# Performance work log

Hardware: AMD Instinct MI355X
Metric: run time of the kernel (lower is better)

## Reference

```python
import jax, jax.numpy as jnp
import numpy as np

B, C, H, W = 4, 256, 64, 64
N = H * W


def setup_inputs() -> dict:
    key = jax.random.key(0)
    k1, k2, k3, k4, k5 = jax.random.split(key, 5)
    energy = jax.random.normal(k1, (B, N, N), dtype=jnp.float32)
    x = jax.random.normal(k2, (B, C, H, W), dtype=jnp.float32)
    # 1x1 conv params (kernel is [C_out, C_in] after squeezing the 1x1 spatial dims)
    fan = 1.0 / np.sqrt(C)
    value_w = jax.random.uniform(k3, (C, C), dtype=jnp.float32, minval=-fan, maxval=fan)
    value_b = jax.random.uniform(k4, (C,), dtype=jnp.float32, minval=-fan, maxval=fan)
    # nn.Parameter(torch.zeros(1)) -> use small random scalar so output is non-trivial
    gamma = jax.random.normal(k5, (1,), dtype=jnp.float32) * 0.1
    return {"energy": energy, "x": x, "value_w": value_w, "value_b": value_b, "gamma": gamma}


def reference(energy, x, value_w, value_b, gamma):
    # softmax over last dim of the [B, N, N] score matrix (dropout in eval mode = identity)
    attention = jax.nn.softmax(energy, axis=-1)  # [B, N, N]
    # 1x1 conv: per-pixel channel mixing
    value = jnp.einsum('bchw,oc->bohw', x, value_w) + value_b[None, :, None, None]
    value = value.reshape(x.shape[0], -1, N)  # [B, C, N]
    # out[b,c,m] = sum_n value[b,c,n] * attention[b,m,n]  (bmm with attention^T)
    out = jnp.einsum('bcn,bmn->bcm', value, attention)
    out = out.reshape(x.shape)  # [B, C, H, W]
    return gamma[0] * out + 2.0 * x
```

## Files before the change

### kernel.cpp

```cpp
#include <hip/hip_runtime.h>

#define Bb 4
#define Cc 256
#define Nn 4096

typedef __attribute__((ext_vector_type(8))) short bf16x8;
typedef __attribute__((ext_vector_type(4))) float f32x4;

__device__ __forceinline__ unsigned short f2bf(float f) {
    union { float f; unsigned u; } v; v.f = f;
    unsigned r = v.u + 0x7FFF + ((v.u >> 16) & 1);
    return (unsigned short)(r >> 16);
}

__device__ __forceinline__ void async_copy16(const void* g, void* l) {
    __builtin_amdgcn_global_load_lds(
        (const __attribute__((address_space(1))) unsigned int*)g,
        (__attribute__((address_space(3))) unsigned int*)l, 16, 0, 0);
}

__global__ __launch_bounds__(256) void value_gemm(
    const float* __restrict__ X, const float* __restrict__ W,
    const float* __restrict__ bias, unsigned short* __restrict__ Vout)
{
    __shared__ unsigned short a_lds[128 * 32];
    __shared__ unsigned short b_lds[128 * 32];

    const int t = threadIdx.x;
    const int blk = blockIdx.x;
    const int b  = blk >> 6;
    const int r  = blk & 63;
    const int o0 = (r >> 5) * 128;
    const int n0 = (r & 31) * 128;

    const int wave = t >> 6, lane = t & 63;
    const int wm = wave >> 1, wn = wave & 1;
    const int lrow = lane & 15, lq = lane >> 4;

    f32x4 acc[4][4] = {};

    for (int c0 = 0; c0 < Cc; c0 += 32) {
        __syncthreads();
        #pragma unroll
        for (int k = 0; k < 4; ++k) {
            const int idx = t + 256 * k;
            const int row = idx >> 3, c4 = idx & 7;
            const float4 v = *(const float4*)&W[(size_t)(o0 + row) * Cc + c0 + c4 * 4];
            ushort4 h; h.x = f2bf(v.x); h.y = f2bf(v.y); h.z = f2bf(v.z); h.w = f2bf(v.w);
            *(ushort4*)&a_lds[row * 32 + c4 * 4] = h;
        }
        #pragma unroll
        for (int k = 0; k < 4; ++k) {
            const int idx = t + 256 * k;
            const int rc = idx >> 5, n4 = idx & 31;
            const float4 v = *(const float4*)&X[((size_t)(b * Cc + c0 + rc)) * Nn + n0 + n4 * 4];
            b_lds[(n4 * 4 + 0) * 32 + rc] = f2bf(v.x);
            b_lds[(n4 * 4 + 1) * 32 + rc] = f2bf(v.y);
            b_lds[(n4 * 4 + 2) * 32 + rc] = f2bf(v.z);
            b_lds[(n4 * 4 + 3) * 32 + rc] = f2bf(v.w);
        }
        __syncthreads();

        bf16x8 af[4], bfr[4];
        #pragma unroll
        for (int i = 0; i < 4; ++i)
            af[i] = *(const bf16x8*)&a_lds[(wm * 64 + i * 16 + lrow) * 32 + lq * 8];
        #pragma unroll
        for (int i = 0; i < 4; ++i)
            bfr[i] = *(const bf16x8*)&b_lds[(wn * 64 + i * 16 + lrow) * 32 + lq * 8];
        #pragma unroll
        for (int mi = 0; mi < 4; ++mi)
            #pragma unroll
            for (int ni = 0; ni < 4; ++ni)
                acc[mi][ni] = __builtin_amdgcn_mfma_f32_16x16x32_bf16(
                    af[mi], bfr[ni], acc[mi][ni], 0, 0, 0);
    }

    #pragma unroll
    for (int mi = 0; mi < 4; ++mi) {
        #pragma unroll
        for (int ni = 0; ni < 4; ++ni) {
            #pragma unroll
            for (int rr = 0; rr < 4; ++rr) {
                const int o = o0 + wm * 64 + mi * 16 + lq * 4 + rr;
                const int n = n0 + wn * 64 + ni * 16 + lrow;
                Vout[((size_t)(b * Cc + o)) * Nn + n] = f2bf(acc[mi][ni][rr] + bias[o]);
            }
        }
    }
}

__global__ __launch_bounds__(256) void attn_gemm(
    const unsigned short* __restrict__ V, const float* __restrict__ E,
    const float* __restrict__ X, const float* __restrict__ gamma,
    float* __restrict__ Out)
{
    __shared__ unsigned short a_lds[128 * 32];
    __shared__ unsigned short b_lds[128 * 32];
    __shared__ float sum_lds[128];

    const int t = threadIdx.x;
    const int blk = blockIdx.x;
    const int b  = blk >> 6;
    const int r  = blk & 63;
    const int c0 = (r >> 5) * 128;
    const int m0 = (r & 31) * 128;

    const int wave = t >> 6, lane = t & 63;
    const int wm = wave >> 1, wn = wave & 1;
    const int lrow = lane & 15, lq = lane >> 4;

    f32x4 acc[4][4] = {};
    float sacc[4] = {0.f, 0.f, 0.f, 0.f};

    const int arow0 = t >> 2;
    const int acol  = (t & 3) * 8;

    for (int k0 = 0; k0 < Nn; k0 += 32) {
        __syncthreads();
        async_copy16(&V[((size_t)(b * Cc + c0 + arow0)) * Nn + k0 + acol],
                     &a_lds[(size_t)t * 8]);
        async_copy16(&V[((size_t)(b * Cc + c0 + 64 + arow0)) * Nn + k0 + acol],
                     &a_lds[(size_t)(t + 256) * 8]);
        #pragma unroll
        for (int k = 0; k < 4; ++k) {
            const int idx = t + 256 * k;
            const int rowm = idx >> 3, n4 = idx & 7;
            const float4 e = *(const float4*)&E[((size_t)b * Nn + m0 + rowm) * Nn + k0 + n4 * 4];
            const float e0 = __expf(e.x), e1 = __expf(e.y), e2 = __expf(e.z), e3 = __expf(e.w);
            sacc[k] += (e0 + e1) + (e2 + e3);
            ushort4 h; h.x = f2bf(e0); h.y = f2bf(e1); h.z = f2bf(e2); h.w = f2bf(e3);
            *(ushort4*)&b_lds[rowm * 32 + n4 * 4] = h;
        }
        __syncthreads();

        bf16x8 af[4], bfr[4];
        #pragma unroll
        for (int i = 0; i < 4; ++i)
            af[i] = *(const bf16x8*)&a_lds[(wm * 64 + i * 16 + lrow) * 32 + lq * 8];
        #pragma unroll
        for (int i = 0; i < 4; ++i)
            bfr[i] = *(const bf16x8*)&b_lds[(wn * 64 + i * 16 + lrow) * 32 + lq * 8];
        #pragma unroll
        for (int mi = 0; mi < 4; ++mi)
            #pragma unroll
            for (int ni = 0; ni < 4; ++ni)
                acc[mi][ni] = __builtin_amdgcn_mfma_f32_16x16x32_bf16(
                    af[mi], bfr[ni], acc[mi][ni], 0, 0, 0);
    }

    #pragma unroll
    for (int k = 0; k < 4; ++k) {
        float s = sacc[k];
        s += __shfl_xor(s, 1);
        s += __shfl_xor(s, 2);
        s += __shfl_xor(s, 4);
        if ((t & 7) == 0) sum_lds[(t >> 3) + 32 * k] = s;
    }
    __syncthreads();

    const float g = gamma[0];
    #pragma unroll
    for (int ni = 0; ni < 4; ++ni) {
        const int mloc = wn * 64 + ni * 16 + lrow;
        const float scale = g / sum_lds[mloc];
        const int m = m0 + mloc;
        #pragma unroll
        for (int mi = 0; mi < 4; ++mi) {
            #pragma unroll
            for (int rr = 0; rr < 4; ++rr) {
                const int c = c0 + wm * 64 + mi * 16 + lq * 4 + rr;
                const size_t off = ((size_t)(b * Cc + c)) * Nn + m;
                Out[off] = scale * acc[mi][ni][rr] + 2.0f * X[off];
            }
        }
    }
}

extern "C" void kernel_launch(void* const* d_in, const int* in_sizes, int n_in,
                              void* d_out, int out_size, void* d_ws, size_t ws_size,
                              hipStream_t stream) {
    const float* energy  = (const float*)d_in[0];
    const float* x       = (const float*)d_in[1];
    const float* value_w = (const float*)d_in[2];
    const float* value_b = (const float*)d_in[3];
    const float* gamma   = (const float*)d_in[4];
    float* out = (float*)d_out;
    unsigned short* Vws = (unsigned short*)d_ws;

    value_gemm<<<256, 256, 0, stream>>>(x, value_w, value_b, Vws);
    attn_gemm<<<256, 256, 0, stream>>>(Vws, energy, x, gamma, out);
}
```

Measured before the change: 501.2 us.

## Read energy once per block with full-channel tiles and register-prefetched V pipeline

The attention GEMM now assigns each 512-thread block all 256 channels for 64 output rows, so the large energy matrix is read and exponentiated only once instead of once per channel tile. V fragments are prefetched from global memory directly into registers two steps ahead, and exp'd energy goes into a double-buffered, XOR-swizzled LDS tile with a single barrier per iteration. The value GEMM uses a 64-deep K step with swizzled LDS and smaller output tiles. Trade-offs are higher register pressure and repeated V reads from L2 across blocks.

```diff
diff --git a/kernel.cpp b/kernel.cpp
--- a/kernel.cpp
+++ b/kernel.cpp
@@ -13,165 +13,222 @@
     return (unsigned short)(r >> 16);
 }
 
-__device__ __forceinline__ void async_copy16(const void* g, void* l) {
-    __builtin_amdgcn_global_load_lds(
-        (const __attribute__((address_space(1))) unsigned int*)g,
-        (__attribute__((address_space(3))) unsigned int*)l, 16, 0, 0);
-}
-
 __global__ __launch_bounds__(256) void value_gemm(
     const float* __restrict__ X, const float* __restrict__ W,
     const float* __restrict__ bias, unsigned short* __restrict__ Vout)
 {
-    __shared__ unsigned short a_lds[128 * 32];
-    __shared__ unsigned short b_lds[128 * 32];
+    __shared__ unsigned short a_lds[128 * 64];
+    __shared__ unsigned short b_lds[64 * 64];
 
     const int t = threadIdx.x;
-    const int blk = blockIdx.x;
-    const int b  = blk >> 6;
-    const int r  = blk & 63;
-    const int o0 = (r >> 5) * 128;
-    const int n0 = (r & 31) * 128;
+    const int b  = blockIdx.x >> 7;
+    const int r  = blockIdx.x & 127;
+    const int o0 = (r >> 6) << 7;
+    const int n0 = (r & 63) << 6;
 
     const int wave = t >> 6, lane = t & 63;
     const int wm = wave >> 1, wn = wave & 1;
     const int lrow = lane & 15, lq = lane >> 4;
 
-    f32x4 acc[4][4] = {};
-
-    for (int c0 = 0; c0 < Cc; c0 += 32) {
-        __syncthreads();
-        #pragma unroll
-        for (int k = 0; k < 4; ++k) {
-            const int idx = t + 256 * k;
-            const int row = idx >> 3, c4 = idx & 7;
-            const float4 v = *(const float4*)&W[(size_t)(o0 + row) * Cc + c0 + c4 * 4];
+    f32x4 acc[4][2] = {};
+
+    for (int c0 = 0; c0 < Cc; c0 += 64) {
+        __syncthreads();
+        #pragma unroll
+        for (int j = 0; j < 8; ++j) {
+            const int q = t + 256 * j;
+            const int row = q >> 4, f = q & 15;
+            const float4 v = *(const float4*)&W[(size_t)(o0 + row) * Cc + c0 + f * 4];
             ushort4 h; h.x = f2bf(v.x); h.y = f2bf(v.y); h.z = f2bf(v.z); h.w = f2bf(v.w);
-            *(ushort4*)&a_lds[row * 32 + c4 * 4] = h;
-        }
-        #pragma unroll
-        for (int k = 0; k < 4; ++k) {
-            const int idx = t + 256 * k;
-            const int rc = idx >> 5, n4 = idx & 31;
-            const float4 v = *(const float4*)&X[((size_t)(b * Cc + c0 + rc)) * Nn + n0 + n4 * 4];
-            b_lds[(n4 * 4 + 0) * 32 + rc] = f2bf(v.x);
-            b_lds[(n4 * 4 + 1) * 32 + rc] = f2bf(v.y);
-            b_lds[(n4 * 4 + 2) * 32 + rc] = f2bf(v.z);
-            b_lds[(n4 * 4 + 3) * 32 + rc] = f2bf(v.w);
-        }
-        __syncthreads();
-
-        bf16x8 af[4], bfr[4];
-        #pragma unroll
-        for (int i = 0; i < 4; ++i)
-            af[i] = *(const bf16x8*)&a_lds[(wm * 64 + i * 16 + lrow) * 32 + lq * 8];
-        #pragma unroll
-        for (int i = 0; i < 4; ++i)
-            bfr[i] = *(const bf16x8*)&b_lds[(wn * 64 + i * 16 + lrow) * 32 + lq * 8];
-        #pragma unroll
-        for (int mi = 0; mi < 4; ++mi)
-            #pragma unroll
-            for (int ni = 0; ni < 4; ++ni)
-                acc[mi][ni] = __builtin_amdgcn_mfma_f32_16x16x32_bf16(
-                    af[mi], bfr[ni], acc[mi][ni], 0, 0, 0);
+            const int addr = row * 64 + (((f >> 1) ^ (row & 7)) << 3) + ((f & 1) << 2);
+            *(ushort4*)&a_lds[addr] = h;
+        }
+        #pragma unroll
+        for (int j = 0; j < 4; ++j) {
+            const int q = t + 256 * j;
+            const int cc = q >> 4, f = q & 15;
+            const float4 v = *(const float4*)&X[((size_t)(b * Cc + c0 + cc)) * Nn + n0 + f * 4];
+            const float vv[4] = {v.x, v.y, v.z, v.w};
+            #pragma unroll
+            for (int e = 0; e < 4; ++e) {
+                const int nn = f * 4 + e;
+                b_lds[nn * 64 + (((cc >> 3) ^ (nn & 7)) << 3) + (cc & 7)] = f2bf(vv[e]);
+            }
+        }
+        __syncthreads();
+
+        bf16x8 af[2][4], bfr[2][2];
+        #pragma unroll
+        for (int kk = 0; kk < 2; ++kk) {
+            #pragma unroll
+            for (int oi = 0; oi < 4; ++oi) {
+                const int row = wm * 64 + oi * 16 + lrow;
+                af[kk][oi] = *(const bf16x8*)&a_lds[row * 64 + (((kk * 4 + lq) ^ (lrow & 7)) << 3)];
+            }
+            #pragma unroll
+            for (int ni = 0; ni < 2; ++ni) {
+                const int rn = wn * 32 + ni * 16 + lrow;
+                bfr[kk][ni] = *(const bf16x8*)&b_lds[rn * 64 + (((kk * 4 + lq) ^ (lrow & 7)) << 3)];
+            }
+        }
+        #pragma unroll
+        for (int oi = 0; oi < 4; ++oi)
+            #pragma unroll
+            for (int ni = 0; ni < 2; ++ni)
+                #pragma unroll
+                for (int kk = 0; kk < 2; ++kk)
+                    acc[oi][ni] = __builtin_amdgcn_mfma_f32_16x16x32_bf16(
+                        af[kk][oi], bfr[kk][ni], acc[oi][ni], 0, 0, 0);
     }
 
     #pragma unroll
-    for (int mi = 0; mi < 4; ++mi) {
-        #pragma unroll
-        for (int ni = 0; ni < 4; ++ni) {
+    for (int oi = 0; oi < 4; ++oi) {
+        #pragma unroll
+        for (int ni = 0; ni < 2; ++ni) {
             #pragma unroll
             for (int rr = 0; rr < 4; ++rr) {
-                const int o = o0 + wm * 64 + mi * 16 + lq * 4 + rr;
-                const int n = n0 + wn * 64 + ni * 16 + lrow;
-                Vout[((size_t)(b * Cc + o)) * Nn + n] = f2bf(acc[mi][ni][rr] + bias[o]);
-            }
-        }
-    }
-}
-
-__global__ __launch_bounds__(256) void attn_gemm(
+                const int o = o0 + wm * 64 + oi * 16 + lq * 4 + rr;
+                const int n = n0 + wn * 32 + ni * 16 + lrow;
+                Vout[((size_t)(b * Cc + o)) * Nn + n] = f2bf(acc[oi][ni][rr] + bias[o]);
+            }
+        }
+    }
+}
+
+__global__ __launch_bounds__(512, 2) void attn_gemm(
     const unsigned short* __restrict__ V, const float* __restrict__ E,
     const float* __restrict__ X, const float* __restrict__ gamma,
     float* __restrict__ Out)
 {
-    __shared__ unsigned short a_lds[128 * 32];
-    __shared__ unsigned short b_lds[128 * 32];
-    __shared__ float sum_lds[128];
+    __shared__ unsigned short b_lds[2][64 * 64];
+    __shared__ float sum_lds[64];
 
     const int t = threadIdx.x;
-    const int blk = blockIdx.x;
-    const int b  = blk >> 6;
-    const int r  = blk & 63;
-    const int c0 = (r >> 5) * 128;
-    const int m0 = (r & 31) * 128;
+    const int b  = blockIdx.x >> 6;
+    const int m0 = (blockIdx.x & 63) << 6;
 
     const int wave = t >> 6, lane = t & 63;
     const int wm = wave >> 1, wn = wave & 1;
     const int lrow = lane & 15, lq = lane >> 4;
 
-    f32x4 acc[4][4] = {};
-    float sacc[4] = {0.f, 0.f, 0.f, 0.f};
-
-    const int arow0 = t >> 2;
-    const int acol  = (t & 3) * 8;
-
-    for (int k0 = 0; k0 < Nn; k0 += 32) {
-        __syncthreads();
-        async_copy16(&V[((size_t)(b * Cc + c0 + arow0)) * Nn + k0 + acol],
-                     &a_lds[(size_t)t * 8]);
-        async_copy16(&V[((size_t)(b * Cc + c0 + 64 + arow0)) * Nn + k0 + acol],
-                     &a_lds[(size_t)(t + 256) * 8]);
-        #pragma unroll
-        for (int k = 0; k < 4; ++k) {
-            const int idx = t + 256 * k;
-            const int rowm = idx >> 3, n4 = idx & 7;
-            const float4 e = *(const float4*)&E[((size_t)b * Nn + m0 + rowm) * Nn + k0 + n4 * 4];
-            const float e0 = __expf(e.x), e1 = __expf(e.y), e2 = __expf(e.z), e3 = __expf(e.w);
-            sacc[k] += (e0 + e1) + (e2 + e3);
-            ushort4 h; h.x = f2bf(e0); h.y = f2bf(e1); h.z = f2bf(e2); h.w = f2bf(e3);
-            *(ushort4*)&b_lds[rowm * 32 + n4 * 4] = h;
-        }
-        __syncthreads();
-
-        bf16x8 af[4], bfr[4];
-        #pragma unroll
-        for (int i = 0; i < 4; ++i)
-            af[i] = *(const bf16x8*)&a_lds[(wm * 64 + i * 16 + lrow) * 32 + lq * 8];
-        #pragma unroll
-        for (int i = 0; i < 4; ++i)
-            bfr[i] = *(const bf16x8*)&b_lds[(wn * 64 + i * 16 + lrow) * 32 + lq * 8];
-        #pragma unroll
-        for (int mi = 0; mi < 4; ++mi)
-            #pragma unroll
-            for (int ni = 0; ni < 4; ++ni)
-                acc[mi][ni] = __builtin_amdgcn_mfma_f32_16x16x32_bf16(
-                    af[mi], bfr[ni], acc[mi][ni], 0, 0, 0);
-    }
-
+    const int rowm = t >> 3;
+    const int n4   = t & 7;
+    const float* Ebase = E + (size_t)b * Nn * Nn + (size_t)(m0 + rowm) * Nn + n4 * 4;
+    const unsigned short* Vb = V + (size_t)b * Cc * Nn;
+
+    const int st0 = rowm * 64 + (((n4 >> 1) ^ (rowm & 7)) << 3) + ((n4 & 1) << 2);
+    const int st1 = rowm * 64 + (((4 + (n4 >> 1)) ^ (rowm & 7)) << 3) + ((n4 & 1) << 2);
+
+    size_t vrow[4];
     #pragma unroll
-    for (int k = 0; k < 4; ++k) {
-        float s = sacc[k];
+    for (int ci = 0; ci < 4; ++ci)
+        vrow[ci] = (size_t)(wm * 64 + ci * 16 + lrow) * Nn + lq * 8;
+
+    f32x4 acc[4][2] = {};
+    float sacc = 0.f;
+
+    bf16x8 vcur[2][4], vnext[2][4];
+    float4 ena, enb;
+
+    {
+        float4 ea0 = *(const float4*)(Ebase + 0);
+        float4 eb0 = *(const float4*)(Ebase + 32);
+        #pragma unroll
+        for (int kk = 0; kk < 2; ++kk)
+            #pragma unroll
+            for (int ci = 0; ci < 4; ++ci)
+                vcur[kk][ci] = *(const bf16x8*)(Vb + vrow[ci] + kk * 32);
+        ena = *(const float4*)(Ebase + 64);
+        enb = *(const float4*)(Ebase + 96);
+        #pragma unroll
+        for (int kk = 0; kk < 2; ++kk)
+            #pragma unroll
+            for (int ci = 0; ci < 4; ++ci)
+                vnext[kk][ci] = *(const bf16x8*)(Vb + vrow[ci] + 64 + kk * 32);
+        const float e0 = __expf(ea0.x), e1 = __expf(ea0.y), e2 = __expf(ea0.z), e3 = __expf(ea0.w);
+        const float e4 = __expf(eb0.x), e5 = __expf(eb0.y), e6 = __expf(eb0.z), e7 = __expf(eb0.w);
+        sacc += ((e0 + e1) + (e2 + e3)) + ((e4 + e5) + (e6 + e7));
+        ushort4 h0; h0.x = f2bf(e0); h0.y = f2bf(e1); h0.z = f2bf(e2); h0.w = f2bf(e3);
+        ushort4 h1; h1.x = f2bf(e4); h1.y = f2bf(e5); h1.z = f2bf(e6); h1.w = f2bf(e7);
+        *(ushort4*)&b_lds[0][st0] = h0;
+        *(ushort4*)&b_lds[0][st1] = h1;
+        __syncthreads();
+    }
+
+    #pragma unroll 2
+    for (int k = 0; k < 64; ++k) {
+        const int cur = k & 1;
+        const int kx2 = ((k + 2) << 6) & (Nn - 1);
+
+        float4 e2a = *(const float4*)(Ebase + kx2);
+        float4 e2b = *(const float4*)(Ebase + kx2 + 32);
+        bf16x8 v2[2][4];
+        #pragma unroll
+        for (int kk = 0; kk < 2; ++kk)
+            #pragma unroll
+            for (int ci = 0; ci < 4; ++ci)
+                v2[kk][ci] = *(const bf16x8*)(Vb + vrow[ci] + kx2 + kk * 32);
+
+        if (k < 63) {
+            const float e0 = __expf(ena.x), e1 = __expf(ena.y), e2 = __expf(ena.z), e3 = __expf(ena.w);
+            const float e4 = __expf(enb.x), e5 = __expf(enb.y), e6 = __expf(enb.z), e7 = __expf(enb.w);
+            sacc += ((e0 + e1) + (e2 + e3)) + ((e4 + e5) + (e6 + e7));
+            ushort4 h0; h0.x = f2bf(e0); h0.y = f2bf(e1); h0.z = f2bf(e2); h0.w = f2bf(e3);
+            ushort4 h1; h1.x = f2bf(e4); h1.y = f2bf(e5); h1.z = f2bf(e6); h1.w = f2bf(e7);
+            *(ushort4*)&b_lds[cur ^ 1][st0] = h0;
+            *(ushort4*)&b_lds[cur ^ 1][st1] = h1;
+        }
+
+        bf16x8 bfr[2][2];
+        #pragma unroll
+        for (int kk = 0; kk < 2; ++kk)
+            #pragma unroll
+            for (int mi = 0; mi < 2; ++mi) {
+                const int rm = wn * 32 + mi * 16 + lrow;
+                bfr[kk][mi] = *(const bf16x8*)&b_lds[cur][rm * 64 + (((kk * 4 + lq) ^ (lrow & 7)) << 3)];
+            }
+        #pragma unroll
+        for (int ci = 0; ci < 4; ++ci)
+            #pragma unroll
+            for (int mi = 0; mi < 2; ++mi)
+                #pragma unroll
+                for (int kk = 0; kk < 2; ++kk)
+                    acc[ci][mi] = __builtin_amdgcn_mfma_f32_16x16x32_bf16(
+                        vcur[kk][ci], bfr[kk][mi], acc[ci][mi], 0, 0, 0);
+
+        #pragma unroll
+        for (int kk = 0; kk < 2; ++kk)
+            #pragma unroll
+            for (int ci = 0; ci < 4; ++ci) {
+                vcur[kk][ci] = vnext[kk][ci];
+                vnext[kk][ci] = v2[kk][ci];
+            }
+        ena = e2a; enb = e2b;
+        __syncthreads();
+    }
+
+    {
+        float s = sacc;
         s += __shfl_xor(s, 1);
         s += __shfl_xor(s, 2);
         s += __shfl_xor(s, 4);
-        if ((t & 7) == 0) sum_lds[(t >> 3) + 32 * k] = s;
+        if (n4 == 0) sum_lds[rowm] = s;
     }
     __syncthreads();
 
     const float g = gamma[0];
     #pragma unroll
-    for (int ni = 0; ni < 4; ++ni) {
-        const int mloc = wn * 64 + ni * 16 + lrow;
+    for (int mi = 0; mi < 2; ++mi) {
+        const int mloc = wn * 32 + mi * 16 + lrow;
         const float scale = g / sum_lds[mloc];
         const int m = m0 + mloc;
         #pragma unroll
-        for (int mi = 0; mi < 4; ++mi) {
+        for (int ci = 0; ci < 4; ++ci) {
             #pragma unroll
             for (int rr = 0; rr < 4; ++rr) {
-                const int c = c0 + wm * 64 + mi * 16 + lq * 4 + rr;
+                const int c = wm * 64 + ci * 16 + lq * 4 + rr;
                 const size_t off = ((size_t)(b * Cc + c)) * Nn + m;
-                Out[off] = scale * acc[mi][ni][rr] + 2.0f * X[off];
+                Out[off] = scale * acc[ci][mi][rr] + 2.0f * X[off];
             }
         }
     }
@@ -188,6 +245,6 @@
     float* out = (float*)d_out;
     unsigned short* Vws = (unsigned short*)d_ws;
 
-    value_gemm<<<256, 256, 0, stream>>>(x, value_w, value_b, Vws);
-    attn_gemm<<<256, 256, 0, stream>>>(Vws, energy, x, gamma, out);
-}
+    value_gemm<<<512, 256, 0, stream>>>(x, value_w, value_b, Vws);
+    attn_gemm<<<256, 512, 0, stream>>>(Vws, energy, x, gamma, out);
+}
```

After: 469.0 us. 6.4% less time.

## Drop LDS staging; load MFMA fragments directly from global with register prefetch

Applied to the files above, without the earlier changes.

Both GEMM kernels stop staging tiles through shared memory. Each wave now loads its bf16 MFMA fragments straight from global memory into registers. In attn_gemm, each block covers all 256 channels for 32 rows of m, so each energy row is read and exponentiated exactly once rather than by two channel blocks. The loop software-prefetches energy two steps ahead and V one step ahead, row sums are reduced with shuffles instead of LDS, and the grid grows to 512 blocks with batch-interleaved block ordering. In exchange, global loads become less coalesced (16-32 byte fragments per lane, strided scalar X loads in value_gemm) and register pressure rises.

```diff
diff --git a/kernel.cpp b/kernel.cpp
--- a/kernel.cpp
+++ b/kernel.cpp
@@ -1,8 +1,8 @@
 #include <hip/hip_runtime.h>
 
-#define Bb 4
+#define Nn 4096
 #define Cc 256
-#define Nn 4096
+#define NN2 ((size_t)Nn * Nn)
 
 typedef __attribute__((ext_vector_type(8))) short bf16x8;
 typedef __attribute__((ext_vector_type(4))) float f32x4;
@@ -13,78 +13,64 @@
     return (unsigned short)(r >> 16);
 }
 
-__device__ __forceinline__ void async_copy16(const void* g, void* l) {
-    __builtin_amdgcn_global_load_lds(
-        (const __attribute__((address_space(1))) unsigned int*)g,
-        (__attribute__((address_space(3))) unsigned int*)l, 16, 0, 0);
+__device__ __forceinline__ bf16x8 pack2(const float4& a, const float4& b) {
+    bf16x8 o;
+    o[0] = (short)f2bf(a.x); o[1] = (short)f2bf(a.y);
+    o[2] = (short)f2bf(a.z); o[3] = (short)f2bf(a.w);
+    o[4] = (short)f2bf(b.x); o[5] = (short)f2bf(b.y);
+    o[6] = (short)f2bf(b.z); o[7] = (short)f2bf(b.w);
+    return o;
 }
 
 __global__ __launch_bounds__(256) void value_gemm(
     const float* __restrict__ X, const float* __restrict__ W,
     const float* __restrict__ bias, unsigned short* __restrict__ Vout)
 {
-    __shared__ unsigned short a_lds[128 * 32];
-    __shared__ unsigned short b_lds[128 * 32];
-
     const int t = threadIdx.x;
-    const int blk = blockIdx.x;
-    const int b  = blk >> 6;
-    const int r  = blk & 63;
-    const int o0 = (r >> 5) * 128;
-    const int n0 = (r & 31) * 128;
-
+    const int b  = blockIdx.x >> 7;
+    const int n0 = (blockIdx.x & 127) << 5;
     const int wave = t >> 6, lane = t & 63;
-    const int wm = wave >> 1, wn = wave & 1;
     const int lrow = lane & 15, lq = lane >> 4;
 
-    f32x4 acc[4][4] = {};
-
-    for (int c0 = 0; c0 < Cc; c0 += 32) {
-        __syncthreads();
-        #pragma unroll
-        for (int k = 0; k < 4; ++k) {
-            const int idx = t + 256 * k;
-            const int row = idx >> 3, c4 = idx & 7;
-            const float4 v = *(const float4*)&W[(size_t)(o0 + row) * Cc + c0 + c4 * 4];
-            ushort4 h; h.x = f2bf(v.x); h.y = f2bf(v.y); h.z = f2bf(v.z); h.w = f2bf(v.w);
-            *(ushort4*)&a_lds[row * 32 + c4 * 4] = h;
-        }
-        #pragma unroll
-        for (int k = 0; k < 4; ++k) {
-            const int idx = t + 256 * k;
-            const int rc = idx >> 5, n4 = idx & 31;
-            const float4 v = *(const float4*)&X[((size_t)(b * Cc + c0 + rc)) * Nn + n0 + n4 * 4];
-            b_lds[(n4 * 4 + 0) * 32 + rc] = f2bf(v.x);
-            b_lds[(n4 * 4 + 1) * 32 + rc] = f2bf(v.y);
-            b_lds[(n4 * 4 + 2) * 32 + rc] = f2bf(v.z);
-            b_lds[(n4 * 4 + 3) * 32 + rc] = f2bf(v.w);
-        }
-        __syncthreads();
-
-        bf16x8 af[4], bfr[4];
-        #pragma unroll
-        for (int i = 0; i < 4; ++i)
-            af[i] = *(const bf16x8*)&a_lds[(wm * 64 + i * 16 + lrow) * 32 + lq * 8];
-        #pragma unroll
-        for (int i = 0; i < 4; ++i)
-            bfr[i] = *(const bf16x8*)&b_lds[(wn * 64 + i * 16 + lrow) * 32 + lq * 8];
-        #pragma unroll
-        for (int mi = 0; mi < 4; ++mi)
-            #pragma unroll
-            for (int ni = 0; ni < 4; ++ni)
-                acc[mi][ni] = __builtin_amdgcn_mfma_f32_16x16x32_bf16(
-                    af[mi], bfr[ni], acc[mi][ni], 0, 0, 0);
-    }
-
-    #pragma unroll
-    for (int mi = 0; mi < 4; ++mi) {
-        #pragma unroll
-        for (int ni = 0; ni < 4; ++ni) {
-            #pragma unroll
-            for (int rr = 0; rr < 4; ++rr) {
-                const int o = o0 + wm * 64 + mi * 16 + lq * 4 + rr;
-                const int n = n0 + wn * 64 + ni * 16 + lrow;
-                Vout[((size_t)(b * Cc + o)) * Nn + n] = f2bf(acc[mi][ni][rr] + bias[o]);
+    const float* Xb = X + (size_t)b * Cc * Nn;
+    f32x4 acc[4][2] = {};
+
+    #pragma unroll 2
+    for (int k0 = 0; k0 < Cc; k0 += 32) {
+        bf16x8 af[4];
+        #pragma unroll
+        for (int ci = 0; ci < 4; ++ci) {
+            const float* wp = W + (size_t)(wave * 64 + ci * 16 + lrow) * Cc + k0 + lq * 8;
+            af[ci] = pack2(*(const float4*)wp, *(const float4*)(wp + 4));
+        }
+        bf16x8 bp[2];
+        #pragma unroll
+        for (int mi = 0; mi < 2; ++mi) {
+            const int n = n0 + mi * 16 + lrow;
+            const float* xp = Xb + (size_t)(k0 + lq * 8) * Nn + n;
+            bf16x8 o;
+            #pragma unroll
+            for (int j = 0; j < 8; ++j) o[j] = (short)f2bf(xp[(size_t)j * Nn]);
+            bp[mi] = o;
+        }
+        #pragma unroll
+        for (int ci = 0; ci < 4; ++ci)
+            #pragma unroll
+            for (int mi = 0; mi < 2; ++mi)
+                acc[ci][mi] = __builtin_amdgcn_mfma_f32_16x16x32_bf16(
+                    af[ci], bp[mi], acc[ci][mi], 0, 0, 0);
+    }
+
+    #pragma unroll
+    for (int ci = 0; ci < 4; ++ci) {
+        #pragma unroll
+        for (int rr = 0; rr < 4; ++rr) {
+            const int o = wave * 64 + ci * 16 + lq * 4 + rr;
+            const float bo = bias[o];
+            #pragma unroll
+            for (int mi = 0; mi < 2; ++mi) {
+                const int n = n0 + mi * 16 + lrow;
+                Vout[((size_t)(b * Cc + o)) * Nn + n] = f2bf(acc[ci][mi][rr] + bo);
             }
         }
     }
@@ -95,83 +81,104 @@
     const float* __restrict__ X, const float* __restrict__ gamma,
     float* __restrict__ Out)
 {
-    __shared__ unsigned short a_lds[128 * 32];
-    __shared__ unsigned short b_lds[128 * 32];
-    __shared__ float sum_lds[128];
-
     const int t = threadIdx.x;
     const int blk = blockIdx.x;
-    const int b  = blk >> 6;
-    const int r  = blk & 63;
-    const int c0 = (r >> 5) * 128;
-    const int m0 = (r & 31) * 128;
+    const int b  = (blk >> 1) & 3;
+    const int mt = ((blk >> 3) << 1) + (blk & 1);
+    const int m0 = mt << 5;
 
     const int wave = t >> 6, lane = t & 63;
-    const int wm = wave >> 1, wn = wave & 1;
     const int lrow = lane & 15, lq = lane >> 4;
 
-    f32x4 acc[4][4] = {};
-    float sacc[4] = {0.f, 0.f, 0.f, 0.f};
-
-    const int arow0 = t >> 2;
-    const int acol  = (t & 3) * 8;
-
-    for (int k0 = 0; k0 < Nn; k0 += 32) {
-        __syncthreads();
-        async_copy16(&V[((size_t)(b * Cc + c0 + arow0)) * Nn + k0 + acol],
-                     &a_lds[(size_t)t * 8]);
-        async_copy16(&V[((size_t)(b * Cc + c0 + 64 + arow0)) * Nn + k0 + acol],
-                     &a_lds[(size_t)(t + 256) * 8]);
-        #pragma unroll
-        for (int k = 0; k < 4; ++k) {
-            const int idx = t + 256 * k;
-            const int rowm = idx >> 3, n4 = idx & 7;
-            const float4 e = *(const float4*)&E[((size_t)b * Nn + m0 + rowm) * Nn + k0 + n4 * 4];
-            const float e0 = __expf(e.x), e1 = __expf(e.y), e2 = __expf(e.z), e3 = __expf(e.w);
-            sacc[k] += (e0 + e1) + (e2 + e3);
-            ushort4 h; h.x = f2bf(e0); h.y = f2bf(e1); h.z = f2bf(e2); h.w = f2bf(e3);
-            *(ushort4*)&b_lds[rowm * 32 + n4 * 4] = h;
-        }
-        __syncthreads();
-
-        bf16x8 af[4], bfr[4];
-        #pragma unroll
-        for (int i = 0; i < 4; ++i)
-            af[i] = *(const bf16x8*)&a_lds[(wm * 64 + i * 16 + lrow) * 32 + lq * 8];
-        #pragma unroll
-        for (int i = 0; i < 4; ++i)
-            bfr[i] = *(const bf16x8*)&b_lds[(wn * 64 + i * 16 + lrow) * 32 + lq * 8];
-        #pragma unroll
-        for (int mi = 0; mi < 4; ++mi)
-            #pragma unroll
-            for (int ni = 0; ni < 4; ++ni)
-                acc[mi][ni] = __builtin_amdgcn_mfma_f32_16x16x32_bf16(
-                    af[mi], bfr[ni], acc[mi][ni], 0, 0, 0);
-    }
-
-    #pragma unroll
-    for (int k = 0; k < 4; ++k) {
-        float s = sacc[k];
-        s += __shfl_xor(s, 1);
-        s += __shfl_xor(s, 2);
-        s += __shfl_xor(s, 4);
-        if ((t & 7) == 0) sum_lds[(t >> 3) + 32 * k] = s;
-    }
-    __syncthreads();
+    const unsigned short* vp[4];
+    #pragma unroll
+    for (int ci = 0; ci < 4; ++ci)
+        vp[ci] = V + ((size_t)(b * Cc + wave * 64 + ci * 16 + lrow)) * Nn + lq * 8;
+    const float* ep[2];
+    #pragma unroll
+    for (int mi = 0; mi < 2; ++mi)
+        ep[mi] = E + (size_t)b * NN2 + (size_t)(m0 + mi * 16 + lrow) * Nn + lq * 8;
+
+    f32x4 acc[4][2] = {};
+    float sacc[2] = {0.f, 0.f};
+
+    float4 e0[2][2], e1[2][2];
+    bf16x8 a0[4];
+    #pragma unroll
+    for (int mi = 0; mi < 2; ++mi) {
+        e0[mi][0] = *(const float4*)(ep[mi]);
+        e0[mi][1] = *(const float4*)(ep[mi] + 4);
+        e1[mi][0] = *(const float4*)(ep[mi] + 32);
+        e1[mi][1] = *(const float4*)(ep[mi] + 36);
+    }
+    #pragma unroll
+    for (int ci = 0; ci < 4; ++ci) a0[ci] = *(const bf16x8*)(vp[ci]);
+
+    #pragma unroll 2
+    for (int k = 0; k < 128; ++k) {
+        const int ko2 = ((k + 2) & 127) << 5;
+        const int ko1 = ((k + 1) & 127) << 5;
+
+        float4 en[2][2];
+        #pragma unroll
+        for (int mi = 0; mi < 2; ++mi) {
+            en[mi][0] = *(const float4*)(ep[mi] + ko2);
+            en[mi][1] = *(const float4*)(ep[mi] + ko2 + 4);
+        }
+        bf16x8 an[4];
+        #pragma unroll
+        for (int ci = 0; ci < 4; ++ci) an[ci] = *(const bf16x8*)(vp[ci] + ko1);
+
+        bf16x8 bp[2];
+        #pragma unroll
+        for (int mi = 0; mi < 2; ++mi) {
+            const float s0 = __expf(e0[mi][0].x), s1 = __expf(e0[mi][0].y),
+                        s2 = __expf(e0[mi][0].z), s3 = __expf(e0[mi][0].w),
+                        s4 = __expf(e0[mi][1].x), s5 = __expf(e0[mi][1].y),
+                        s6 = __expf(e0[mi][1].z), s7 = __expf(e0[mi][1].w);
+            sacc[mi] += ((s0 + s1) + (s2 + s3)) + ((s4 + s5) + (s6 + s7));
+            bf16x8 o;
+            o[0] = (short)f2bf(s0); o[1] = (short)f2bf(s1);
+            o[2] = (short)f2bf(s2); o[3] = (short)f2bf(s3);
+            o[4] = (short)f2bf(s4); o[5] = (short)f2bf(s5);
+            o[6] = (short)f2bf(s6); o[7] = (short)f2bf(s7);
+            bp[mi] = o;
+        }
+
+        #pragma unroll
+        for (int ci = 0; ci < 4; ++ci)
+            #pragma unroll
+            for (int mi = 0; mi < 2; ++mi)
+                acc[ci][mi] = __builtin_amdgcn_mfma_f32_16x16x32_bf16(
+                    a0[ci], bp[mi], acc[ci][mi], 0, 0, 0);
+
+        #pragma unroll
+        for (int mi = 0; mi < 2; ++mi) {
+            e0[mi][0] = e1[mi][0]; e0[mi][1] = e1[mi][1];
+            e1[mi][0] = en[mi][0]; e1[mi][1] = en[mi][1];
+        }
+        #pragma unroll
+        for (int ci = 0; ci < 4; ++ci) a0[ci] = an[ci];
+    }
+
+    #pragma unroll
+    for (int mi = 0; mi < 2; ++mi) {
+        sacc[mi] += __shfl_xor(sacc[mi], 16);
+        sacc[mi] += __shfl_xor(sacc[mi], 32);
+    }
 
     const float g = gamma[0];
     #pragma unroll
-    for (int ni = 0; ni < 4; ++ni) {
-        const int mloc = wn * 64 + ni * 16 + lrow;
-        const float scale = g / sum_lds[mloc];
-        const int m = m0 + mloc;
-        #pragma unroll
-        for (int mi = 0; mi < 4; ++mi) {
+    for (int mi = 0; mi < 2; ++mi) {
+        const float scale = g / sacc[mi];
+        const int m = m0 + mi * 16 + lrow;
+        #pragma unroll
+        for (int ci = 0; ci < 4; ++ci) {
             #pragma unroll
             for (int rr = 0; rr < 4; ++rr) {
-                const int c = c0 + wm * 64 + mi * 16 + lq * 4 + rr;
+                const int c = wave * 64 + ci * 16 + lq * 4 + rr;
                 const size_t off = ((size_t)(b * Cc + c)) * Nn + m;
-                Out[off] = scale * acc[mi][ni][rr] + 2.0f * X[off];
+                Out[off] = scale * acc[ci][mi][rr] + 2.0f * X[off];
             }
         }
     }
@@ -188,6 +195,6 @@
     float* out = (float*)d_out;
     unsigned short* Vws = (unsigned short*)d_ws;
 
-    value_gemm<<<256, 256, 0, stream>>>(x, value_w, value_b, Vws);
-    attn_gemm<<<256, 256, 0, stream>>>(Vws, energy, x, gamma, out);
-}
+    value_gemm<<<512, 256, 0, stream>>>(x, value_w, value_b, Vws);
+    attn_gemm<<<512, 256, 0, stream>>>(Vws, energy, x, gamma, out);
+}
```

Result: slower. 718.4 us (+43.3%).
